# Kernel tuning notes

Hardware: AMD Instinct MI355X
Metric: run time of the kernel (lower is better)

Reference implementation:

```python
import jax, jax.numpy as jnp
import numpy as np

N_QUBITS = 6
N_QLAYERS = 3
CNOT = jnp.array([[1,0,0,0],[0,1,0,0],[0,0,0,1],[0,0,1,0]], dtype=jnp.complex64).reshape(2,2,2,2)


def _rx(t):
    c = jnp.cos(0.5 * t).astype(jnp.complex64)
    s = jnp.sin(0.5 * t).astype(jnp.complex64)
    return jnp.stack([jnp.stack([c, -1j * s]), jnp.stack([-1j * s, c])])


def _ry(t):
    c = jnp.cos(0.5 * t).astype(jnp.complex64)
    s = jnp.sin(0.5 * t).astype(jnp.complex64)
    return jnp.stack([jnp.stack([c, -s]), jnp.stack([s, c])])


def _rz(t):
    e0 = jnp.exp(-0.5j * t)
    e1 = jnp.exp(0.5j * t)
    z = jnp.zeros((), jnp.complex64)
    return jnp.stack([jnp.stack([e0, z]), jnp.stack([z, e1])])


def _apply1(state, U, wire):
    st = jnp.tensordot(U, state, axes=([1], [wire]))
    return jnp.moveaxis(st, 0, wire)


def _apply_cnot(state, c, t):
    st = jnp.tensordot(CNOT, state, axes=([2, 3], [c, t]))
    return jnp.moveaxis(st, (0, 1), (c, t))


def _circuit(inputs, weights):
    # 6-qubit statevector sim of the PennyLane circuit; inputs: [6], weights: [3,6]
    state = jnp.zeros((2,) * N_QUBITS, jnp.complex64).at[(0,) * N_QUBITS].set(1.0)
    for i in range(N_QUBITS):
        state = _apply1(state, _rx(inputs[i % N_QUBITS]), i)
        state = _apply1(state, _ry(inputs[(i + 1) % N_QUBITS]), i)
        state = _apply1(state, _rz(inputs[(i + 2) % N_QUBITS]), i)
    for _l in range(N_QLAYERS):
        for q in range(N_QUBITS):
            state = _apply1(state, _ry(weights[_l, q]), q)
        for q in range(N_QUBITS):
            state = _apply_cnot(state, q, (q + 1) % N_QUBITS)
    probs = jnp.abs(state) ** 2
    zvec = jnp.array([1.0, -1.0], jnp.float32)
    return jnp.stack([jnp.tensordot(probs, zvec, axes=([i], [0])).sum() for i in range(N_QUBITS)])


def _forward(x, cw1, cb1, cw2, cb2, cw3, cb3, W_ih, W_hh, b_ih, b_hh, q_weights, Wq, bq, Wo, bo):
    h = jnp.transpose(x, (0, 2, 1))  # [B, F, T]
    for W, b in ((cw1, cb1), (cw2, cb2), (cw3, cb3)):
        h = jax.lax.conv_general_dilated(h, W, (1,), [(1, 1)], dimension_numbers=('NCH', 'OIH', 'NCH')) + b[None, :, None]
        h = jax.nn.relu(h)
    tcn_out = jnp.transpose(h, (0, 2, 1))  # [B, T, H]
    B, H = x.shape[0], tcn_out.shape[2]
    qbatch = jax.vmap(lambda inp: _circuit(inp, q_weights))

    def step(carry, x_t):
        hx, cx = carry
        gates = x_t @ W_ih.T + b_ih + hx @ W_hh.T + b_hh
        i_g, f_g, g_g, o_g = jnp.split(gates, 4, axis=1)
        c = jax.nn.sigmoid(f_g) * cx + jax.nn.sigmoid(i_g) * jnp.tanh(g_g)
        hh = jax.nn.sigmoid(o_g) * jnp.tanh(c)
        hh = 3.99 * hh * (1.0 - hh)  # logistic map
        x_new = 1.0 - 1.4 * hh[:, 0] ** 2 + hh[:, 1]  # henon map on dims 0,1
        y_new = 0.3 * hh[:, 0]
        hh = jnp.concatenate([x_new[:, None], y_new[:, None], hh[:, 2:]], axis=1)
        q = qbatch(hh[:, :N_QUBITS])  # [B, 6]
        hh = hh + q @ Wq.T + bq  # QuantumRNNCell(hx, hx)
        return (hh, c), None

    step = jax.checkpoint(step)
    hx = jnp.zeros((B, H), x.dtype)
    cx = jnp.zeros((B, H), x.dtype)
    (hx, cx), _ = jax.lax.scan(step, (hx, cx), jnp.swapaxes(tcn_out, 0, 1))
    return jax.nn.sigmoid(hx @ Wo.T + bo)  # [B, 1]


def setup_inputs() -> dict:
    key = jax.random.key(0)
    ks = jax.random.split(key, 20)
    B, T, F, H = 4096, 256, 32, 32

    def u(k, shape, fan):
        s = 1.0 / np.sqrt(fan)
        return jax.random.uniform(k, shape, jnp.float32, -s, s)

    return {
        'x': jax.random.normal(ks[0], (B, T, F), jnp.float32),
        'cw1': u(ks[1], (H, F, 3), F * 3), 'cb1': u(ks[2], (H,), F * 3),
        'cw2': u(ks[3], (H, H, 3), H * 3), 'cb2': u(ks[4], (H,), H * 3),
        'cw3': u(ks[5], (H, H, 3), H * 3), 'cb3': u(ks[6], (H,), H * 3),
        'W_ih': u(ks[7], (4 * H, H), H), 'W_hh': u(ks[8], (4 * H, H), H),
        'b_ih': u(ks[9], (4 * H,), H), 'b_hh': u(ks[10], (4 * H,), H),
        'q_weights': jax.random.uniform(ks[11], (N_QLAYERS, N_QUBITS), jnp.float32, 0.0, 2.0 * np.pi),
        'Wq': u(ks[12], (H, N_QUBITS), N_QUBITS), 'bq': u(ks[13], (H,), N_QUBITS),
        'Wo': u(ks[14], (1, H), H), 'bo': u(ks[15], (1,), H),
    }


def reference(x, cw1, cb1, cw2, cb2, cw3, cb3, W_ih, W_hh, b_ih, b_hh, q_weights, Wq, bq, Wo, bo):
    return _forward(x, cw1, cb1, cw2, cb2, cw3, cb3, W_ih, W_hh, b_ih, b_hh, q_weights, Wq, bq, Wo, bo)
```

## Files before the change

kernel.cpp:

```cpp
#include <hip/hip_runtime.h>

#define B_TOT 4096
#define T_LEN 256
#define NCH   32

typedef float f2 __attribute__((ext_vector_type(2)));
typedef float f4 __attribute__((ext_vector_type(4)));

__device__ __forceinline__ float rdlane(float v, int l) {
    return __int_as_float(__builtin_amdgcn_readlane(__float_as_int(v), l));
}
__device__ __forceinline__ float xor1f(float x) {
    return __int_as_float(__builtin_amdgcn_mov_dpp(__float_as_int(x), 0xB1, 0xF, 0xF, true));
}
__device__ __forceinline__ float xor2f(float x) {
    return __int_as_float(__builtin_amdgcn_mov_dpp(__float_as_int(x), 0x4E, 0xF, 0xF, true));
}
__device__ __forceinline__ float xor3f(float x) {
    return __int_as_float(__builtin_amdgcn_mov_dpp(__float_as_int(x), 0x1B, 0xF, 0xF, true));
}
__device__ __forceinline__ float xor8f(float x) {
    return __int_as_float(__builtin_amdgcn_mov_dpp(__float_as_int(x), 0x128, 0xF, 0xF, true));
}
__device__ __forceinline__ float xsign(float x, unsigned m) {
    return __int_as_float(__float_as_int(x) ^ (int)m);
}
__device__ __forceinline__ float fast_sig(float x) {
    return __builtin_amdgcn_rcpf(1.0f + __expf(-x));
}
__device__ __forceinline__ float fast_tanh(float x) {
    return fmaf(-2.0f, __builtin_amdgcn_rcpf(__expf(2.0f * x) + 1.0f), 1.0f);
}

__device__ __forceinline__ void fast_sincos(float x, float& s, float& c) {
    float k = rintf(x * 0.3183098861837907f);
    float r = fmaf(-k, 3.14159274101257324f, x);
    r = fmaf(-k, -8.74227765734758577e-8f, r);
    float r2 = r * r;
    float sp = fmaf(-2.50521084e-8f, r2, 2.75573192e-6f);
    sp = fmaf(sp, r2, -1.98412698e-4f);
    sp = fmaf(sp, r2, 8.33333333e-3f);
    sp = fmaf(sp, r2, -1.66666667e-1f);
    float sv = fmaf(sp * r2, r, r);
    float cp = fmaf(2.08767570e-9f, r2, -2.75573192e-7f);
    cp = fmaf(cp, r2, 2.48015873e-5f);
    cp = fmaf(cp, r2, -1.38888889e-3f);
    cp = fmaf(cp, r2, 4.16666667e-2f);
    cp = fmaf(cp, r2, -0.5f);
    float cv = fmaf(cp, r2, 1.0f);
    float sgn = ((int)k & 1) ? -1.0f : 1.0f;
    s = sv * sgn;
    c = cv * sgn;
}

__device__ __forceinline__ void sincos_poly(float x, float& s, float& c) {
    float r2 = x * x;
    float sp = fmaf(-2.50521084e-8f, r2, 2.75573192e-6f);
    sp = fmaf(sp, r2, -1.98412698e-4f);
    sp = fmaf(sp, r2, 8.33333333e-3f);
    sp = fmaf(sp, r2, -1.66666667e-1f);
    s = fmaf(sp * r2, x, x);
    float cp = fmaf(2.08767570e-9f, r2, -2.75573192e-7f);
    cp = fmaf(cp, r2, 2.48015873e-5f);
    cp = fmaf(cp, r2, -1.38888889e-3f);
    cp = fmaf(cp, r2, 4.16666667e-2f);
    cp = fmaf(cp, r2, -0.5f);
    c = fmaf(cp, r2, 1.0f);
}

__global__ __launch_bounds__(256) void tcn_kernel(
    const float* __restrict__ x,
    const float* __restrict__ cw1, const float* __restrict__ cb1,
    const float* __restrict__ cw2, const float* __restrict__ cb2,
    const float* __restrict__ cw3, const float* __restrict__ cb3,
    float* __restrict__ out)
{
    __shared__ float bufA[NCH * 258];
    __shared__ float bufB[NCH * 258];
    __shared__ float sW[NCH * 97];
    __shared__ float sB[NCH];

    const int b   = blockIdx.x;
    const int tid = threadIdx.x;
    const float* xb = x + (size_t)b * T_LEN * NCH;

    #pragma unroll
    for (int c = 0; c < 32; ++c) {
        int idx = c * 256 + tid;
        int t = idx >> 5, f = idx & 31;
        bufA[f * 258 + t] = xb[idx];
    }
    __syncthreads();

    float* bin  = bufA;
    float* bout = bufB;
    const int o  = tid & 31;
    const int t0 = (tid >> 5) * 32;

    for (int layer = 0; layer < 3; ++layer) {
        const float* Wg = (layer == 0) ? cw1 : ((layer == 1) ? cw2 : cw3);
        const float* Bg = (layer == 0) ? cb1 : ((layer == 1) ? cb2 : cb3);
        for (int idx = tid; idx < 32 * 96; idx += 256) {
            int oo = idx / 96, rem = idx - oo * 96;
            sW[oo * 97 + rem] = Wg[idx];
        }
        if (tid < 32) sB[tid] = Bg[tid];
        __syncthreads();

        f2 acc2[16];
        const float bias = sB[o];
        #pragma unroll
        for (int j = 0; j < 16; ++j) acc2[j] = f2{bias, bias};

        for (int i = 0; i < 32; ++i) {
            const float w0 = sW[o * 97 + i * 3 + 0];
            const float w1 = sW[o * 97 + i * 3 + 1];
            const float w2 = sW[o * 97 + i * 3 + 2];
            const float* row = bin + i * 258;
            const f2* rp = (const f2*)(row + t0);
            float vmE = (t0 == 0)   ? 0.0f : row[t0 - 1];
            float vpE = (t0 == 224) ? 0.0f : row[t0 + 32];
            f2 Lprev = f2{0.0f, 0.0f};
            f2 Lcur  = rp[0];
            #pragma unroll
            for (int j = 0; j < 16; ++j) {
                f2 Lnext = (j < 15) ? rp[j + 1] : f2{vpE, 0.0f};
                f2 vm = (j == 0) ? f2{vmE, Lcur.x}
                                 : __builtin_shufflevector(Lprev, Lcur, 1, 2);
                f2 vp = __builtin_shufflevector(Lcur, Lnext, 1, 2);
                acc2[j] = __builtin_elementwise_fma(f2{w0, w0}, vm,   acc2[j]);
                acc2[j] = __builtin_elementwise_fma(f2{w1, w1}, Lcur, acc2[j]);
                acc2[j] = __builtin_elementwise_fma(f2{w2, w2}, vp,   acc2[j]);
                Lprev = Lcur; Lcur = Lnext;
            }
        }
        f2* wout = (f2*)(bout + o * 258 + t0);
        #pragma unroll
        for (int j = 0; j < 16; ++j) {
            f2 r;
            r.x = fmaxf(acc2[j].x, 0.0f);
            r.y = fmaxf(acc2[j].y, 0.0f);
            wout[j] = r;
        }
        __syncthreads();
        float* tmp = bin; bin = bout; bout = tmp;
    }

    float* og = out + (size_t)b * T_LEN * NCH;
    #pragma unroll
    for (int c = 0; c < 32; ++c) {
        int idx = c * 256 + tid;
        int t = idx >> 5, f = idx & 31;
        og[idx] = bin[f * 258 + t];
    }
}

__global__ __launch_bounds__(64, 2) void scan_kernel(
    const float* __restrict__ tcn,
    const float* __restrict__ W_ih, const float* __restrict__ W_hh,
    const float* __restrict__ b_ih, const float* __restrict__ b_hh,
    const float* __restrict__ qw,
    const float* __restrict__ Wq, const float* __restrict__ bq,
    const float* __restrict__ Wo, const float* __restrict__ bo,
    float* __restrict__ out)
{
    __shared__ __align__(16) float hb[64];

    const int lane = threadIdx.x;
    const int b2   = blockIdx.x * 2;
    const float* xrowA = tcn + (size_t)b2 * T_LEN * NCH;
    const float* xrowB = xrowA + T_LEN * NCH;

    f2 wih[32], whh[32];
    #pragma unroll
    for (int k = 0; k < 32; ++k) {
        wih[k] = f2{ W_ih[lane * 32 + k], W_ih[(lane + 64) * 32 + k] };
        whh[k] = f2{ W_hh[lane * 32 + k], W_hh[(lane + 64) * 32 + k] };
    }
    const f2 bias01 = f2{ b_ih[lane] + b_hh[lane],
                          b_ih[lane + 64] + b_hh[lane + 64] };

    float ssu[18], ccu[18];
    {
        float s0, c0;
        int j = (lane < 18) ? lane : 0;
        fast_sincos(0.5f * qw[j], s0, c0);
        #pragma unroll
        for (int i = 0; i < 18; ++i) { ssu[i] = rdlane(s0, i); ccu[i] = rdlane(c0, i); }
    }
    float vs1 = ssu[0], vc1 = ccu[0];
    #pragma unroll
    for (int i = 1; i < 6; ++i) {
        vs1 = (lane == i) ? ssu[i] : vs1;
        vc1 = (lane == i) ? ccu[i] : vc1;
    }
    const int MU2[6] = {31, 48, 56, 60, 62, 63};
    const int MU3[6] = {53, 47, 23, 43, 21, 42};
    float ssl2[6], ssl3[6], cc2[6], cc3[6];
    #pragma unroll
    for (int q = 0; q < 6; ++q) {
        ssl2[q] = (__popc(lane & MU2[q]) & 1) ? ssu[6 + q]  : -ssu[6 + q];
        ssl3[q] = (__popc(lane & MU3[q]) & 1) ? ssu[12 + q] : -ssu[12 + q];
        cc2[q] = ccu[6 + q];
        cc3[q] = ccu[12 + q];
    }
    unsigned nm[6];
    #pragma unroll
    for (int q = 0; q < 6; ++q) nm[q] = (lane & (32 >> q)) ? 0u : 0x80000000u;
    const int r1 = (lane + 1) % 6, r2 = (lane + 2) % 6;

    float wqr[6] = {0, 0, 0, 0, 0, 0};
    float bqr = 0.0f, wor = 0.0f;
    if (lane < 32) {
        #pragma unroll
        for (int k = 0; k < 6; ++k) wqr[k] = Wq[lane * 6 + k];
        bqr = bq[lane];
        wor = Wo[lane];
    }

    float hhA = 0.0f, cellA = 0.0f, hhB = 0.0f, cellB = 0.0f;
    const f4* hq = (const f4*)hb;

    for (int t = 0; t < T_LEN; ++t) {
        if (lane < 32) ((f2*)hb)[lane] = f2{hhA, hhB};
        const float* xA = xrowA + t * 32;
        const float* xB = xrowB + t * 32;

        f2 aA = bias01, bA_ = f2{0.0f, 0.0f};
        f2 aB = bias01, bB_ = f2{0.0f, 0.0f};
        #pragma unroll
        for (int j = 0; j < 16; ++j) {
            f4 hv = hq[j];
            float x0A = xA[2 * j], x1A = xA[2 * j + 1];
            float x0B = xB[2 * j], x1B = xB[2 * j + 1];
            aA  = __builtin_elementwise_fma(wih[2*j],   f2{x0A, x0A},   aA);
            aA  = __builtin_elementwise_fma(whh[2*j],   f2{hv.x, hv.x}, aA);
            bA_ = __builtin_elementwise_fma(wih[2*j+1], f2{x1A, x1A},   bA_);
            bA_ = __builtin_elementwise_fma(whh[2*j+1], f2{hv.z, hv.z}, bA_);
            aB  = __builtin_elementwise_fma(wih[2*j],   f2{x0B, x0B},   aB);
            aB  = __builtin_elementwise_fma(whh[2*j],   f2{hv.y, hv.y}, aB);
            bB_ = __builtin_elementwise_fma(wih[2*j+1], f2{x1B, x1B},   bB_);
            bB_ = __builtin_elementwise_fma(whh[2*j+1], f2{hv.w, hv.w}, bB_);
        }
        aA += bA_; aB += bB_;
        float acc0A = aA.x, acc1A = aA.y;
        float acc0B = aB.x, acc1B = aB.y;

        float fgA = __shfl_xor(acc0A, 32, 64), ogA = __shfl_xor(acc1A, 32, 64);
        float fgB = __shfl_xor(acc0B, 32, 64), ogB = __shfl_xor(acc1B, 32, 64);
        float cA = fast_sig(fgA) * cellA + fast_sig(acc0A) * fast_tanh(acc1A);
        float cB = fast_sig(fgB) * cellB + fast_sig(acc0B) * fast_tanh(acc1B);
        float hA = fast_sig(ogA) * fast_tanh(cA);
        float hB = fast_sig(ogB) * fast_tanh(cB);
        hA = 3.99f * hA * (1.0f - hA);
        hB = 3.99f * hB * (1.0f - hB);
        float h0A = rdlane(hA, 0), h1A = rdlane(hA, 1);
        float h0B = rdlane(hB, 0), h1B = rdlane(hB, 1);
        float henA0 = fmaf(-1.4f * h0A, h0A, 1.0f) + h1A;
        float henB0 = fmaf(-1.4f * h0B, h0B, 1.0f) + h1B;
        hA = (lane == 0) ? henA0 : hA;
        hB = (lane == 0) ? henB0 : hB;
        hA = (lane == 1) ? 0.3f * h0A : hA;
        hB = (lane == 1) ? 0.3f * h0B : hB;
        cellA = cA; cellB = cB;

        float sOA, cOA, sOB, cOB;
        sincos_poly(0.5f * hA, sOA, cOA);
        sincos_poly(0.5f * hB, sOB, cOB);
        float s1A = __shfl(sOA, r1, 64), c1A = __shfl(cOA, r1, 64);
        float s1B = __shfl(sOB, r1, 64), c1B = __shfl(cOB, r1, 64);
        float s2A = __shfl(sOA, r2, 64), c2A = __shfl(cOA, r2, 64);
        float s2B = __shfl(sOB, r2, 64), c2B = __shfl(cOB, r2, 64);
        float nurA, nuiA, nprA, npiA, nurB, nuiB, nprB, npiB;
        {
            float A_ = c1A * cOA, Bv = s1A * sOA;
            float C_ = s1A * cOA, D_ = c1A * sOA;
            float ur = fmaf(Bv, s2A,  A_ * c2A);
            float ui = fmaf(Bv, c2A, -(A_ * s2A));
            float pr = fmaf(D_, s2A,  C_ * c2A);
            float pi = fmaf(C_, s2A, -(D_ * c2A));
            nurA = fmaf(vc1, ur, -(vs1 * pr));
            nuiA = fmaf(vc1, ui, -(vs1 * pi));
            nprA = fmaf(vs1, ur,  vc1 * pr);
            npiA = fmaf(vs1, ui,  vc1 * pi);
        }
        {
            float A_ = c1B * cOB, Bv = s1B * sOB;
            float C_ = s1B * cOB, D_ = c1B * sOB;
            float ur = fmaf(Bv, s2B,  A_ * c2B);
            float ui = fmaf(Bv, c2B, -(A_ * s2B));
            float pr = fmaf(D_, s2B,  C_ * c2B);
            float pi = fmaf(C_, s2B, -(D_ * c2B));
            nurB = fmaf(vc1, ur, -(vs1 * pr));
            nuiB = fmaf(vc1, ui, -(vs1 * pi));
            nprB = fmaf(vs1, ur,  vc1 * pr);
            npiB = fmaf(vs1, ui,  vc1 * pi);
        }

        float reA, imA, reB, imB;
        {
            bool hi0 = (lane & 32) != 0;
            float uA = rdlane(nurA, 0), vA = rdlane(nuiA, 0);
            float pA_ = rdlane(nprA, 0), qA_ = rdlane(npiA, 0);
            float uB = rdlane(nurB, 0), vB = rdlane(nuiB, 0);
            float pB_ = rdlane(nprB, 0), qB_ = rdlane(npiB, 0);
            reA = hi0 ? pA_ : uA;  imA = hi0 ? qA_ : vA;
            reB = hi0 ? pB_ : uB;  imB = hi0 ? qB_ : vB;
        }
        #pragma unroll
        for (int i = 1; i < 6; ++i) {
            const bool hi = (lane & (32 >> i)) != 0;
            float uA = rdlane(nurA, i), vA = rdlane(nuiA, i);
            float pA_ = rdlane(nprA, i), qA_ = rdlane(npiA, i);
            float uB = rdlane(nurB, i), vB = rdlane(nuiB, i);
            float pB_ = rdlane(nprB, i), qB_ = rdlane(npiB, i);
            float grA = hi ? pA_ : uA, giA = hi ? qA_ : vA;
            float grB = hi ? pB_ : uB, giB = hi ? qB_ : vB;
            float nrA = fmaf(reA, grA, -(imA * giA));
            float niA = fmaf(reA, giA,   imA * grA);
            float nrB = fmaf(reB, grB, -(imB * giB));
            float niB = fmaf(reB, giB,   imB * grB);
            reA = nrA; imA = niA; reB = nrB; imB = niB;
        }

        {
            float pA, qA, pB, qB;
            pA = __shfl_xor(reA, 48, 64); qA = __shfl_xor(imA, 48, 64);
            pB = __shfl_xor(reB, 48, 64); qB = __shfl_xor(imB, 48, 64);
            reA = fmaf(ssl2[0], pA, cc2[0] * reA); imA = fmaf(ssl2[0], qA, cc2[0] * imA);
            reB = fmaf(ssl2[0], pB, cc2[0] * reB); imB = fmaf(ssl2[0], qB, cc2[0] * imB);
            pA = __shfl_xor(reA, 24, 64); qA = __shfl_xor(imA, 24, 64);
            pB = __shfl_xor(reB, 24, 64); qB = __shfl_xor(imB, 24, 64);
            reA = fmaf(ssl2[1], pA, cc2[1] * reA); imA = fmaf(ssl2[1], qA, cc2[1] * imA);
            reB = fmaf(ssl2[1], pB, cc2[1] * reB); imB = fmaf(ssl2[1], qB, cc2[1] * imB);
            pA = __shfl_xor(reA, 12, 64); qA = __shfl_xor(imA, 12, 64);
            pB = __shfl_xor(reB, 12, 64); qB = __shfl_xor(imB, 12, 64);
            reA = fmaf(ssl2[2], pA, cc2[2] * reA); imA = fmaf(ssl2[2], qA, cc2[2] * imA);
            reB = fmaf(ssl2[2], pB, cc2[2] * reB); imB = fmaf(ssl2[2], qB, cc2[2] * imB);
            pA = __shfl_xor(reA, 6, 64);  qA = __shfl_xor(imA, 6, 64);
            pB = __shfl_xor(reB, 6, 64);  qB = __shfl_xor(imB, 6, 64);
            reA = fmaf(ssl2[3], pA, cc2[3] * reA); imA = fmaf(ssl2[3], qA, cc2[3] * imA);
            reB = fmaf(ssl2[3], pB, cc2[3] * reB); imB = fmaf(ssl2[3], qB, cc2[3] * imB);
            pA = xor3f(reA); qA = xor3f(imA);
            pB = xor3f(reB); qB = xor3f(imB);
            reA = fmaf(ssl2[4], pA, cc2[4] * reA); imA = fmaf(ssl2[4], qA, cc2[4] * imA);
            reB = fmaf(ssl2[4], pB, cc2[4] * reB); imB = fmaf(ssl2[4], qB, cc2[4] * imB);
            pA = __shfl_xor(reA, 49, 64); qA = __shfl_xor(imA, 49, 64);
            pB = __shfl_xor(reB, 49, 64); qB = __shfl_xor(imB, 49, 64);
            reA = fmaf(ssl2[5], pA, cc2[5] * reA); imA = fmaf(ssl2[5], qA, cc2[5] * imA);
            reB = fmaf(ssl2[5], pB, cc2[5] * reB); imB = fmaf(ssl2[5], qB, cc2[5] * imB);
        }
        {
            float pA, qA, pB, qB;
            pA = __shfl_xor(reA, 40, 64); qA = __shfl_xor(imA, 40, 64);
            pB = __shfl_xor(reB, 40, 64); qB = __shfl_xor(imB, 40, 64);
            reA = fmaf(ssl3[0], pA, cc3[0] * reA); imA = fmaf(ssl3[0], qA, cc3[0] * imA);
            reB = fmaf(ssl3[0], pB, cc3[0] * reB); imB = fmaf(ssl3[0], qB, cc3[0] * imB);
            pA = __shfl_xor(reA, 20, 64); qA = __shfl_xor(imA, 20, 64);
            pB = __shfl_xor(reB, 20, 64); qB = __shfl_xor(imB, 20, 64);
            reA = fmaf(ssl3[1], pA, cc3[1] * reA); imA = fmaf(ssl3[1], qA, cc3[1] * imA);
            reB = fmaf(ssl3[1], pB, cc3[1] * reB); imB = fmaf(ssl3[1], qB, cc3[1] * imB);
            pA = __shfl_xor(reA, 10, 64); qA = __shfl_xor(imA, 10, 64);
            pB = __shfl_xor(reB, 10, 64); qB = __shfl_xor(imB, 10, 64);
            reA = fmaf(ssl3[2], pA, cc3[2] * reA); imA = fmaf(ssl3[2], qA, cc3[2] * imA);
            reB = fmaf(ssl3[2], pB, cc3[2] * reB); imB = fmaf(ssl3[2], qB, cc3[2] * imB);
            pA = __shfl_xor(reA, 5, 64);  qA = __shfl_xor(imA, 5, 64);
            pB = __shfl_xor(reB, 5, 64);  qB = __shfl_xor(imB, 5, 64);
            reA = fmaf(ssl3[3], pA, cc3[3] * reA); imA = fmaf(ssl3[3], qA, cc3[3] * imA);
            reB = fmaf(ssl3[3], pB, cc3[3] * reB); imB = fmaf(ssl3[3], qB, cc3[3] * imB);
            pA = __shfl_xor(reA, 50, 64); qA = __shfl_xor(imA, 50, 64);
            pB = __shfl_xor(reB, 50, 64); qB = __shfl_xor(imB, 50, 64);
            reA = fmaf(ssl3[4], pA, cc3[4] * reA); imA = fmaf(ssl3[4], qA, cc3[4] * imA);
            reB = fmaf(ssl3[4], pB, cc3[4] * reB); imB = fmaf(ssl3[4], qB, cc3[4] * imB);
            pA = __shfl_xor(reA, 25, 64); qA = __shfl_xor(imA, 25, 64);
            pB = __shfl_xor(reB, 25, 64); qB = __shfl_xor(imB, 25, 64);
            reA = fmaf(ssl3[5], pA, cc3[5] * reA); imA = fmaf(ssl3[5], qA, cc3[5] * imA);
            reB = fmaf(ssl3[5], pB, cc3[5] * reB); imB = fmaf(ssl3[5], qB, cc3[5] * imB);
        }

        float pA = fmaf(reA, reA, imA * imA);
        float pB = fmaf(reB, reB, imB * imB);
        { float tA = xor1f(pA), tB = xor1f(pB);
          pA = tA - xsign(pA, nm[5]); pB = tB - xsign(pB, nm[5]); }
        { float tA = xor2f(pA), tB = xor2f(pB);
          pA = tA - xsign(pA, nm[4]); pB = tB - xsign(pB, nm[4]); }
        { float tA = __shfl_xor(pA, 4, 64), tB = __shfl_xor(pB, 4, 64);
          pA = tA - xsign(pA, nm[3]); pB = tB - xsign(pB, nm[3]); }
        { float tA = xor8f(pA), tB = xor8f(pB);
          pA = tA - xsign(pA, nm[2]); pB = tB - xsign(pB, nm[2]); }
        { float tA = __shfl_xor(pA, 16, 64), tB = __shfl_xor(pB, 16, 64);
          pA = tA - xsign(pA, nm[1]); pB = tB - xsign(pB, nm[1]); }
        { float tA = __shfl_xor(pA, 32, 64), tB = __shfl_xor(pB, 32, 64);
          pA = tA - xsign(pA, nm[0]); pB = tB - xsign(pB, nm[0]); }

        float updA = bqr, updB = bqr;
        updA = fmaf(rdlane(pA, 44), wqr[0], updA); updB = fmaf(rdlane(pB, 44), wqr[0], updB);
        updA = fmaf(rdlane(pA, 26), wqr[1], updA); updB = fmaf(rdlane(pB, 26), wqr[1], updB);
        updA = fmaf(rdlane(pA, 13), wqr[2], updA); updB = fmaf(rdlane(pB, 13), wqr[2], updB);
        updA = fmaf(rdlane(pA, 38), wqr[3], updA); updB = fmaf(rdlane(pB, 38), wqr[3], updB);
        updA = fmaf(rdlane(pA, 51), wqr[4], updA); updB = fmaf(rdlane(pB, 51), wqr[4], updB);
        updA = fmaf(rdlane(pA, 25), wqr[5], updA); updB = fmaf(rdlane(pB, 25), wqr[5], updB);
        hhA = hA + updA;
        hhB = hB + updB;
    }

    float cA = (lane < 32) ? hhA * wor : 0.0f;
    float cB = (lane < 32) ? hhB * wor : 0.0f;
    #pragma unroll
    for (int off = 32; off >= 1; off >>= 1) {
        cA += __shfl_xor(cA, off, 64);
        cB += __shfl_xor(cB, off, 64);
    }
    if (lane == 0) {
        float bo0 = bo[0];
        out[b2]     = fast_sig(cA + bo0);
        out[b2 + 1] = fast_sig(cB + bo0);
    }
}

extern "C" void kernel_launch(void* const* d_in, const int* in_sizes, int n_in,
                              void* d_out, int out_size, void* d_ws, size_t ws_size,
                              hipStream_t stream)
{
    const float* x    = (const float*)d_in[0];
    const float* cw1  = (const float*)d_in[1];
    const float* cb1  = (const float*)d_in[2];
    const float* cw2  = (const float*)d_in[3];
    const float* cb2  = (const float*)d_in[4];
    const float* cw3  = (const float*)d_in[5];
    const float* cb3  = (const float*)d_in[6];
    const float* W_ih = (const float*)d_in[7];
    const float* W_hh = (const float*)d_in[8];
    const float* b_ih = (const float*)d_in[9];
    const float* b_hh = (const float*)d_in[10];
    const float* qw   = (const float*)d_in[11];
    const float* Wq   = (const float*)d_in[12];
    const float* bq   = (const float*)d_in[13];
    const float* Wo   = (const float*)d_in[14];
    const float* bo   = (const float*)d_in[15];

    float* tcn = (float*)d_ws;

    hipLaunchKernelGGL(tcn_kernel, dim3(B_TOT), dim3(256), 0, stream,
                       x, cw1, cb1, cw2, cb2, cw3, cb3, tcn);
    hipLaunchKernelGGL(scan_kernel, dim3(B_TOT / 2), dim3(64), 0, stream,
                       tcn, W_ih, W_hh, b_ih, b_hh, qw, Wq, bq, Wo, bo,
                       (float*)d_out);
}
```

Baseline: 1.088 ms.

## Undo CNOT permutation with explicit lane shuffles and stage x through LDS

The quantum layer previously folded each CNOT ring's basis permutation into irregular XOR shuffle masks and popcount sign patterns. It now applies an explicit lane-permutation shuffle after each layer, so the RY stages use standard power-of-two XOR masks, several of them cheap DPP moves. The LSTM input row for the next step is also prefetched into a register one step ahead and written to shared memory alongside the hidden state. This replaces 32 scalar global loads per step with vector LDS reads. The cost is three extra full shuffles (12 bpermutes) per timestep, which adds latency on the serial critical path.

```diff
diff --git a/kernel.cpp b/kernel.cpp
--- a/kernel.cpp
+++ b/kernel.cpp
@@ -15,9 +15,6 @@
 }
 __device__ __forceinline__ float xor2f(float x) {
     return __int_as_float(__builtin_amdgcn_mov_dpp(__float_as_int(x), 0x4E, 0xF, 0xF, true));
-}
-__device__ __forceinline__ float xor3f(float x) {
-    return __int_as_float(__builtin_amdgcn_mov_dpp(__float_as_int(x), 0x1B, 0xF, 0xF, true));
 }
 __device__ __forceinline__ float xor8f(float x) {
     return __int_as_float(__builtin_amdgcn_mov_dpp(__float_as_int(x), 0x128, 0xF, 0xF, true));
@@ -164,7 +161,7 @@
     const float* __restrict__ Wo, const float* __restrict__ bo,
     float* __restrict__ out)
 {
-    __shared__ __align__(16) float hb[64];
+    __shared__ __align__(16) float xcA[64], xcB[64];
 
     const int lane = threadIdx.x;
     const int b2   = blockIdx.x * 2;
@@ -194,19 +191,25 @@
         vs1 = (lane == i) ? ssu[i] : vs1;
         vc1 = (lane == i) ? ccu[i] : vc1;
     }
-    const int MU2[6] = {31, 48, 56, 60, 62, 63};
-    const int MU3[6] = {53, 47, 23, 43, 21, 42};
-    float ssl2[6], ssl3[6], cc2[6], cc3[6];
+    float ss2[6], ss3[6], cc2[6], cc3[6];
     #pragma unroll
     for (int q = 0; q < 6; ++q) {
-        ssl2[q] = (__popc(lane & MU2[q]) & 1) ? ssu[6 + q]  : -ssu[6 + q];
-        ssl3[q] = (__popc(lane & MU3[q]) & 1) ? ssu[12 + q] : -ssu[12 + q];
+        bool hi = (lane & (32 >> q)) != 0;
+        ss2[q] = hi ? ssu[6 + q]  : -ssu[6 + q];
+        ss3[q] = hi ? ssu[12 + q] : -ssu[12 + q];
         cc2[q] = ccu[6 + q];
         cc3[q] = ccu[12 + q];
     }
     unsigned nm[6];
     #pragma unroll
     for (int q = 0; q < 6; ++q) nm[q] = (lane & (32 >> q)) ? 0u : 0x80000000u;
+    int psrc = lane;
+    psrc ^= (psrc & 1) << 5;
+    psrc ^= (psrc & 2) >> 1;
+    psrc ^= (psrc & 4) >> 1;
+    psrc ^= (psrc & 8) >> 1;
+    psrc ^= (psrc & 16) >> 1;
+    psrc ^= (psrc & 32) >> 1;
     const int r1 = (lane + 1) % 6, r2 = (lane + 2) % 6;
 
     float wqr[6] = {0, 0, 0, 0, 0, 0};
@@ -219,28 +222,33 @@
     }
 
     float hhA = 0.0f, cellA = 0.0f, hhB = 0.0f, cellB = 0.0f;
-    const f4* hq = (const f4*)hb;
+    float xpA = (lane < 32) ? xrowA[lane] : 0.0f;
+    float xpB = (lane < 32) ? xrowB[lane] : 0.0f;
+
+    const f4* xqA = (const f4*)xcA;
+    const f4* xqB = (const f4*)xcB;
 
     for (int t = 0; t < T_LEN; ++t) {
-        if (lane < 32) ((f2*)hb)[lane] = f2{hhA, hhB};
-        const float* xA = xrowA + t * 32;
-        const float* xB = xrowB + t * 32;
+        if (lane < 32) {
+            ((f2*)xcA)[lane] = f2{xpA, hhA};
+            ((f2*)xcB)[lane] = f2{xpB, hhB};
+        }
+        float xnA = (lane < 32 && t < T_LEN - 1) ? xrowA[(t + 1) * 32 + lane] : 0.0f;
+        float xnB = (lane < 32 && t < T_LEN - 1) ? xrowB[(t + 1) * 32 + lane] : 0.0f;
 
         f2 aA = bias01, bA_ = f2{0.0f, 0.0f};
         f2 aB = bias01, bB_ = f2{0.0f, 0.0f};
         #pragma unroll
         for (int j = 0; j < 16; ++j) {
-            f4 hv = hq[j];
-            float x0A = xA[2 * j], x1A = xA[2 * j + 1];
-            float x0B = xB[2 * j], x1B = xB[2 * j + 1];
-            aA  = __builtin_elementwise_fma(wih[2*j],   f2{x0A, x0A},   aA);
-            aA  = __builtin_elementwise_fma(whh[2*j],   f2{hv.x, hv.x}, aA);
-            bA_ = __builtin_elementwise_fma(wih[2*j+1], f2{x1A, x1A},   bA_);
-            bA_ = __builtin_elementwise_fma(whh[2*j+1], f2{hv.z, hv.z}, bA_);
-            aB  = __builtin_elementwise_fma(wih[2*j],   f2{x0B, x0B},   aB);
-            aB  = __builtin_elementwise_fma(whh[2*j],   f2{hv.y, hv.y}, aB);
-            bB_ = __builtin_elementwise_fma(wih[2*j+1], f2{x1B, x1B},   bB_);
-            bB_ = __builtin_elementwise_fma(whh[2*j+1], f2{hv.w, hv.w}, bB_);
+            f4 vA = xqA[j], vB = xqB[j];
+            aA  = __builtin_elementwise_fma(wih[2*j],   __builtin_shufflevector(vA, vA, 0, 0), aA);
+            aB  = __builtin_elementwise_fma(wih[2*j],   __builtin_shufflevector(vB, vB, 0, 0), aB);
+            aA  = __builtin_elementwise_fma(whh[2*j],   __builtin_shufflevector(vA, vA, 1, 1), aA);
+            aB  = __builtin_elementwise_fma(whh[2*j],   __builtin_shufflevector(vB, vB, 1, 1), aB);
+            bA_ = __builtin_elementwise_fma(wih[2*j+1], __builtin_shufflevector(vA, vA, 2, 2), bA_);
+            bB_ = __builtin_elementwise_fma(wih[2*j+1], __builtin_shufflevector(vB, vB, 2, 2), bB_);
+            bA_ = __builtin_elementwise_fma(whh[2*j+1], __builtin_shufflevector(vA, vA, 3, 3), bA_);
+            bB_ = __builtin_elementwise_fma(whh[2*j+1], __builtin_shufflevector(vB, vB, 3, 3), bB_);
         }
         aA += bA_; aB += bB_;
         float acc0A = aA.x, acc1A = aA.y;
@@ -323,60 +331,68 @@
             reA = nrA; imA = niA; reB = nrB; imB = niB;
         }
 
+        reA = __shfl(reA, psrc, 64); imA = __shfl(imA, psrc, 64);
+        reB = __shfl(reB, psrc, 64); imB = __shfl(imB, psrc, 64);
+
         {
             float pA, qA, pB, qB;
-            pA = __shfl_xor(reA, 48, 64); qA = __shfl_xor(imA, 48, 64);
-            pB = __shfl_xor(reB, 48, 64); qB = __shfl_xor(imB, 48, 64);
-            reA = fmaf(ssl2[0], pA, cc2[0] * reA); imA = fmaf(ssl2[0], qA, cc2[0] * imA);
-            reB = fmaf(ssl2[0], pB, cc2[0] * reB); imB = fmaf(ssl2[0], qB, cc2[0] * imB);
-            pA = __shfl_xor(reA, 24, 64); qA = __shfl_xor(imA, 24, 64);
-            pB = __shfl_xor(reB, 24, 64); qB = __shfl_xor(imB, 24, 64);
-            reA = fmaf(ssl2[1], pA, cc2[1] * reA); imA = fmaf(ssl2[1], qA, cc2[1] * imA);
-            reB = fmaf(ssl2[1], pB, cc2[1] * reB); imB = fmaf(ssl2[1], qB, cc2[1] * imB);
-            pA = __shfl_xor(reA, 12, 64); qA = __shfl_xor(imA, 12, 64);
-            pB = __shfl_xor(reB, 12, 64); qB = __shfl_xor(imB, 12, 64);
-            reA = fmaf(ssl2[2], pA, cc2[2] * reA); imA = fmaf(ssl2[2], qA, cc2[2] * imA);
-            reB = fmaf(ssl2[2], pB, cc2[2] * reB); imB = fmaf(ssl2[2], qB, cc2[2] * imB);
-            pA = __shfl_xor(reA, 6, 64);  qA = __shfl_xor(imA, 6, 64);
-            pB = __shfl_xor(reB, 6, 64);  qB = __shfl_xor(imB, 6, 64);
-            reA = fmaf(ssl2[3], pA, cc2[3] * reA); imA = fmaf(ssl2[3], qA, cc2[3] * imA);
-            reB = fmaf(ssl2[3], pB, cc2[3] * reB); imB = fmaf(ssl2[3], qB, cc2[3] * imB);
-            pA = xor3f(reA); qA = xor3f(imA);
-            pB = xor3f(reB); qB = xor3f(imB);
-            reA = fmaf(ssl2[4], pA, cc2[4] * reA); imA = fmaf(ssl2[4], qA, cc2[4] * imA);
-            reB = fmaf(ssl2[4], pB, cc2[4] * reB); imB = fmaf(ssl2[4], qB, cc2[4] * imB);
-            pA = __shfl_xor(reA, 49, 64); qA = __shfl_xor(imA, 49, 64);
-            pB = __shfl_xor(reB, 49, 64); qB = __shfl_xor(imB, 49, 64);
-            reA = fmaf(ssl2[5], pA, cc2[5] * reA); imA = fmaf(ssl2[5], qA, cc2[5] * imA);
-            reB = fmaf(ssl2[5], pB, cc2[5] * reB); imB = fmaf(ssl2[5], qB, cc2[5] * imB);
-        }
+            pA = __shfl_xor(reA, 32, 64); qA = __shfl_xor(imA, 32, 64);
+            pB = __shfl_xor(reB, 32, 64); qB = __shfl_xor(imB, 32, 64);
+            reA = fmaf(ss2[0], pA, cc2[0] * reA); imA = fmaf(ss2[0], qA, cc2[0] * imA);
+            reB = fmaf(ss2[0], pB, cc2[0] * reB); imB = fmaf(ss2[0], qB, cc2[0] * imB);
+            pA = __shfl_xor(reA, 16, 64); qA = __shfl_xor(imA, 16, 64);
+            pB = __shfl_xor(reB, 16, 64); qB = __shfl_xor(imB, 16, 64);
+            reA = fmaf(ss2[1], pA, cc2[1] * reA); imA = fmaf(ss2[1], qA, cc2[1] * imA);
+            reB = fmaf(ss2[1], pB, cc2[1] * reB); imB = fmaf(ss2[1], qB, cc2[1] * imB);
+            pA = xor8f(reA); qA = xor8f(imA);
+            pB = xor8f(reB); qB = xor8f(imB);
+            reA = fmaf(ss2[2], pA, cc2[2] * reA); imA = fmaf(ss2[2], qA, cc2[2] * imA);
+            reB = fmaf(ss2[2], pB, cc2[2] * reB); imB = fmaf(ss2[2], qB, cc2[2] * imB);
+            pA = __shfl_xor(reA, 4, 64); qA = __shfl_xor(imA, 4, 64);
+            pB = __shfl_xor(reB, 4, 64); qB = __shfl_xor(imB, 4, 64);
+            reA = fmaf(ss2[3], pA, cc2[3] * reA); imA = fmaf(ss2[3], qA, cc2[3] * imA);
+            reB = fmaf(ss2[3], pB, cc2[3] * reB); imB = fmaf(ss2[3], qB, cc2[3] * imB);
+            pA = xor2f(reA); qA = xor2f(imA);
+            pB = xor2f(reB); qB = xor2f(imB);
+            reA = fmaf(ss2[4], pA, cc2[4] * reA); imA = fmaf(ss2[4], qA, cc2[4] * imA);
+            reB = fmaf(ss2[4], pB, cc2[4] * reB); imB = fmaf(ss2[4], qB, cc2[4] * imB);
+            pA = xor1f(reA); qA = xor1f(imA);
+            pB = xor1f(reB); qB = xor1f(imB);
+            reA = fmaf(ss2[5], pA, cc2[5] * reA); imA = fmaf(ss2[5], qA, cc2[5] * imA);
+            reB = fmaf(ss2[5], pB, cc2[5] * reB); imB = fmaf(ss2[5], qB, cc2[5] * imB);
+        }
+        reA = __shfl(reA, psrc, 64); imA = __shfl(imA, psrc, 64);
+        reB = __shfl(reB, psrc, 64); imB = __shfl(imB, psrc, 64);
+
         {
             float pA, qA, pB, qB;
-            pA = __shfl_xor(reA, 40, 64); qA = __shfl_xor(imA, 40, 64);
-            pB = __shfl_xor(reB, 40, 64); qB = __shfl_xor(imB, 40, 64);
-            reA = fmaf(ssl3[0], pA, cc3[0] * reA); imA = fmaf(ssl3[0], qA, cc3[0] * imA);
-            reB = fmaf(ssl3[0], pB, cc3[0] * reB); imB = fmaf(ssl3[0], qB, cc3[0] * imB);
-            pA = __shfl_xor(reA, 20, 64); qA = __shfl_xor(imA, 20, 64);
-            pB = __shfl_xor(reB, 20, 64); qB = __shfl_xor(imB, 20, 64);
-            reA = fmaf(ssl3[1], pA, cc3[1] * reA); imA = fmaf(ssl3[1], qA, cc3[1] * imA);
-            reB = fmaf(ssl3[1], pB, cc3[1] * reB); imB = fmaf(ssl3[1], qB, cc3[1] * imB);
-            pA = __shfl_xor(reA, 10, 64); qA = __shfl_xor(imA, 10, 64);
-            pB = __shfl_xor(reB, 10, 64); qB = __shfl_xor(imB, 10, 64);
-            reA = fmaf(ssl3[2], pA, cc3[2] * reA); imA = fmaf(ssl3[2], qA, cc3[2] * imA);
-            reB = fmaf(ssl3[2], pB, cc3[2] * reB); imB = fmaf(ssl3[2], qB, cc3[2] * imB);
-            pA = __shfl_xor(reA, 5, 64);  qA = __shfl_xor(imA, 5, 64);
-            pB = __shfl_xor(reB, 5, 64);  qB = __shfl_xor(imB, 5, 64);
-            reA = fmaf(ssl3[3], pA, cc3[3] * reA); imA = fmaf(ssl3[3], qA, cc3[3] * imA);
-            reB = fmaf(ssl3[3], pB, cc3[3] * reB); imB = fmaf(ssl3[3], qB, cc3[3] * imB);
-            pA = __shfl_xor(reA, 50, 64); qA = __shfl_xor(imA, 50, 64);
-            pB = __shfl_xor(reB, 50, 64); qB = __shfl_xor(imB, 50, 64);
-            reA = fmaf(ssl3[4], pA, cc3[4] * reA); imA = fmaf(ssl3[4], qA, cc3[4] * imA);
-            reB = fmaf(ssl3[4], pB, cc3[4] * reB); imB = fmaf(ssl3[4], qB, cc3[4] * imB);
-            pA = __shfl_xor(reA, 25, 64); qA = __shfl_xor(imA, 25, 64);
-            pB = __shfl_xor(reB, 25, 64); qB = __shfl_xor(imB, 25, 64);
-            reA = fmaf(ssl3[5], pA, cc3[5] * reA); imA = fmaf(ssl3[5], qA, cc3[5] * imA);
-            reB = fmaf(ssl3[5], pB, cc3[5] * reB); imB = fmaf(ssl3[5], qB, cc3[5] * imB);
-        }
+            pA = __shfl_xor(reA, 32, 64); qA = __shfl_xor(imA, 32, 64);
+            pB = __shfl_xor(reB, 32, 64); qB = __shfl_xor(imB, 32, 64);
+            reA = fmaf(ss3[0], pA, cc3[0] * reA); imA = fmaf(ss3[0], qA, cc3[0] * imA);
+            reB = fmaf(ss3[0], pB, cc3[0] * reB); imB = fmaf(ss3[0], qB, cc3[0] * imB);
+            pA = __shfl_xor(reA, 16, 64); qA = __shfl_xor(imA, 16, 64);
+            pB = __shfl_xor(reB, 16, 64); qB = __shfl_xor(imB, 16, 64);
+            reA = fmaf(ss3[1], pA, cc3[1] * reA); imA = fmaf(ss3[1], qA, cc3[1] * imA);
+            reB = fmaf(ss3[1], pB, cc3[1] * reB); imB = fmaf(ss3[1], qB, cc3[1] * imB);
+            pA = xor8f(reA); qA = xor8f(imA);
+            pB = xor8f(reB); qB = xor8f(imB);
+            reA = fmaf(ss3[2], pA, cc3[2] * reA); imA = fmaf(ss3[2], qA, cc3[2] * imA);
+            reB = fmaf(ss3[2], pB, cc3[2] * reB); imB = fmaf(ss3[2], qB, cc3[2] * imB);
+            pA = __shfl_xor(reA, 4, 64); qA = __shfl_xor(imA, 4, 64);
+            pB = __shfl_xor(reB, 4, 64); qB = __shfl_xor(imB, 4, 64);
+            reA = fmaf(ss3[3], pA, cc3[3] * reA); imA = fmaf(ss3[3], qA, cc3[3] * imA);
+            reB = fmaf(ss3[3], pB, cc3[3] * reB); imB = fmaf(ss3[3], qB, cc3[3] * imB);
+            pA = xor2f(reA); qA = xor2f(imA);
+            pB = xor2f(reB); qB = xor2f(imB);
+            reA = fmaf(ss3[4], pA, cc3[4] * reA); imA = fmaf(ss3[4], qA, cc3[4] * imA);
+            reB = fmaf(ss3[4], pB, cc3[4] * reB); imB = fmaf(ss3[4], qB, cc3[4] * imB);
+            pA = xor1f(reA); qA = xor1f(imA);
+            pB = xor1f(reB); qB = xor1f(imB);
+            reA = fmaf(ss3[5], pA, cc3[5] * reA); imA = fmaf(ss3[5], qA, cc3[5] * imA);
+            reB = fmaf(ss3[5], pB, cc3[5] * reB); imB = fmaf(ss3[5], qB, cc3[5] * imB);
+        }
+        reA = __shfl(reA, psrc, 64); imA = __shfl(imA, psrc, 64);
+        reB = __shfl(reB, psrc, 64); imB = __shfl(imB, psrc, 64);
 
         float pA = fmaf(reA, reA, imA * imA);
         float pB = fmaf(reB, reB, imB * imB);
@@ -394,14 +410,15 @@
           pA = tA - xsign(pA, nm[0]); pB = tB - xsign(pB, nm[0]); }
 
         float updA = bqr, updB = bqr;
-        updA = fmaf(rdlane(pA, 44), wqr[0], updA); updB = fmaf(rdlane(pB, 44), wqr[0], updB);
-        updA = fmaf(rdlane(pA, 26), wqr[1], updA); updB = fmaf(rdlane(pB, 26), wqr[1], updB);
-        updA = fmaf(rdlane(pA, 13), wqr[2], updA); updB = fmaf(rdlane(pB, 13), wqr[2], updB);
-        updA = fmaf(rdlane(pA, 38), wqr[3], updA); updB = fmaf(rdlane(pB, 38), wqr[3], updB);
-        updA = fmaf(rdlane(pA, 51), wqr[4], updA); updB = fmaf(rdlane(pB, 51), wqr[4], updB);
-        updA = fmaf(rdlane(pA, 25), wqr[5], updA); updB = fmaf(rdlane(pB, 25), wqr[5], updB);
+        updA = fmaf(rdlane(pA, 32), wqr[0], updA); updB = fmaf(rdlane(pB, 32), wqr[0], updB);
+        updA = fmaf(rdlane(pA, 16), wqr[1], updA); updB = fmaf(rdlane(pB, 16), wqr[1], updB);
+        updA = fmaf(rdlane(pA,  8), wqr[2], updA); updB = fmaf(rdlane(pB,  8), wqr[2], updB);
+        updA = fmaf(rdlane(pA,  4), wqr[3], updA); updB = fmaf(rdlane(pB,  4), wqr[3], updB);
+        updA = fmaf(rdlane(pA,  2), wqr[4], updA); updB = fmaf(rdlane(pB,  2), wqr[4], updB);
+        updA = fmaf(rdlane(pA,  1), wqr[5], updA); updB = fmaf(rdlane(pB,  1), wqr[5], updB);
         hhA = hA + updA;
         hhB = hB + updB;
+        xpA = xnA; xpB = xnB;
     }
 
     float cA = (lane < 32) ? hhA * wor : 0.0f;
```

After: 1.125 ms. 1.03x slower.
